# Kernel tuning notes

Measured on AMD Instinct MI355X. Metric: run time of the kernel, lower is better.

## Reference

```python
import jax, jax.numpy as jnp
import numpy as np

WIDTH = 128


def setup_inputs() -> dict:
    key = jax.random.key(0)
    k_logits, k_w1, k_b1, k_w2, k_b2 = jax.random.split(key, 5)
    B, T, V = 32, 256, 4096
    logits = jax.random.normal(k_logits, (B, T, V), dtype=jnp.float32)
    # Linear(1, width): weight [width, 1] -> stored transposed as [1, width]
    w1 = jax.random.normal(k_w1, (1, WIDTH), dtype=jnp.float32) / jnp.sqrt(1.0)
    b1 = jax.random.normal(k_b1, (WIDTH,), dtype=jnp.float32) * 0.1
    # Linear(width, 1): weight [1, width] -> stored transposed as [width, 1]
    w2 = jax.random.normal(k_w2, (WIDTH, 1), dtype=jnp.float32) / jnp.sqrt(WIDTH)
    b2 = jax.random.normal(k_b2, (1,), dtype=jnp.float32) * 0.1
    return {"logits": logits, "w1": w1, "b1": b1, "w2": w2, "b2": b2}


def reference(logits, w1, b1, w2, b2):
    B, T, V = logits.shape
    logits_trim = logits[:, :-1, :]                       # [B, T-1, V]
    # entropy of softmax over the class dim; logits - logsumexp == log_softmax
    logp = jax.nn.log_softmax(logits_trim, axis=-1)       # [B, T-1, V]
    p = jnp.exp(logp)
    entropy = -jnp.sum(p * logp, axis=-1, keepdims=True)  # [B, T-1, 1]
    entropy_max = jnp.log(jnp.asarray(T, dtype=logits.dtype))  # log(num_steps)
    norm = 2.0 * entropy / entropy_max - 1.0              # [B, T-1, 1]
    # tiny 1 -> width -> 1 MLP
    hidden = jax.nn.relu(norm @ w1 + b1)                  # [B, T-1, width]
    lin = (2.0 * hidden) @ w2 + b2                        # [B, T-1, 1]
    # ns = [T-1, T-2, ..., 1]
    ns = jnp.arange(T - 1, 0, -1, dtype=logits.dtype).reshape(1, T - 1, 1)
    flags_trim = jax.nn.sigmoid(lin - jnp.log(ns))        # [B, T-1, 1]
    zeros = jnp.zeros((B, 1, 1), dtype=logits.dtype)
    ones = jnp.ones((B, 1, 1), dtype=logits.dtype)
    flags = jnp.concatenate([zeros, flags_trim, ones], axis=1)  # [B, T+1, 1]
    probabilities = jax.nn.softmax(logits, axis=2)        # [B, T, V]
    residuals = jnp.cumprod(1.0 - flags[:, :-1], axis=1)  # [B, T, 1] survival
    frequencies = probabilities * flags[:, 1:] * residuals  # [B, T, V]
    return frequencies
```

## Files before the change

kernel.cpp:

```cpp
#include <hip/hip_runtime.h>
#include <math.h>

#define T_DIM 256
#define V_DIM 4096
#define WIDTH 128

typedef float floatx4 __attribute__((ext_vector_type(4)));

__device__ __forceinline__ double wave_sum_d(double v) {
#pragma unroll
  for (int o = 32; o > 0; o >>= 1) v += __shfl_xor(v, o);
  return v;
}

__global__ __launch_bounds__(256) void row_stats(
    const float* __restrict__ logits,
    const float* __restrict__ w1, const float* __restrict__ b1,
    const float* __restrict__ w2, const float* __restrict__ b2,
    double* __restrict__ row_Z, double* __restrict__ row_flag) {
  const int wave = threadIdx.x >> 6;
  const int lane = threadIdx.x & 63;
  const int row = blockIdx.x * 4 + wave;
  const int t = row & (T_DIM - 1);

  const float4* src = (const float4*)(logits + (size_t)row * V_DIM);

  float zg[4] = {0.f, 0.f, 0.f, 0.f};
  float sg[4] = {0.f, 0.f, 0.f, 0.f};
#pragma unroll
  for (int k = 0; k < 16; ++k) {
    float4 x = src[lane + k * 64];
    const int g = k & 3;
    float vals[4] = {x.x, x.y, x.z, x.w};
#pragma unroll
    for (int j = 0; j < 4; ++j) {
      float ev = __expf(vals[j]);
      zg[g] += ev;
      sg[g] = fmaf(vals[j], ev, sg[g]);
    }
  }
  double zd = wave_sum_d(((double)zg[0] + (double)zg[1]) +
                         ((double)zg[2] + (double)zg[3]));
  double sd = wave_sum_d(((double)sg[0] + (double)sg[1]) +
                         ((double)sg[2] + (double)sg[3]));

  if (lane == 0) row_Z[row] = zd;

  if (t < T_DIM - 1) {
    double H = (double)__logf((float)zd) - sd / zd;
    double nrm = fma(H, 0.36067376022224085, -1.0);
    double acc = 0.0;
#pragma unroll
    for (int j = lane; j < WIDTH; j += 64) {
      double h = fma(nrm, (double)w1[j], (double)b1[j]);
      h = h > 0.0 ? h : 0.0;
      acc = fma(h, (double)w2[j], acc);
    }
    acc = wave_sum_d(acc);
    if (lane == 0) {
      double lin = 2.0 * acc + (double)b2[0];
      float xx = (float)lin - __logf((float)(T_DIM - 1 - t));
      row_flag[row] = 1.0 / (1.0 + (double)__expf(-xx));
    }
  }
}

__global__ __launch_bounds__(64) void scan_k(
    const double* __restrict__ row_Z, const double* __restrict__ row_flag,
    float* __restrict__ row_scale) {
  const int b = blockIdx.x;
  const int lane = threadIdx.x & 63;
  const double* fb = row_flag + (size_t)b * T_DIM;

  double loc[4];
  double p = 1.0;
#pragma unroll
  for (int j = 0; j < 4; ++j) {
    int t = lane * 4 + j;
    double flag_t = (t == 0) ? 0.0 : fb[t - 1];
    p *= (1.0 - flag_t);
    loc[j] = p;
  }
  double inc = p;
#pragma unroll
  for (int o = 1; o < 64; o <<= 1) {
    double up = __shfl_up(inc, o);
    if (lane >= o) inc *= up;
  }
  double exc = __shfl_up(inc, 1);
  if (lane == 0) exc = 1.0;

#pragma unroll
  for (int j = 0; j < 4; ++j) {
    int t = lane * 4 + j;
    double resid = exc * loc[j];
    double flt = (t == T_DIM - 1) ? 1.0 : fb[t];
    row_scale[(size_t)b * T_DIM + t] =
        (float)(flt * resid / row_Z[(size_t)b * T_DIM + t]);
  }
}

__global__ __launch_bounds__(256) void out_k(const float* __restrict__ logits,
                                             const float* __restrict__ row_scale,
                                             float* __restrict__ out) {
  const int row = blockIdx.x;
  const int tid = threadIdx.x;
  const float sc = row_scale[row];

  const float4* src = (const float4*)(logits + (size_t)row * V_DIM);
  floatx4* dst = (floatx4*)(out + (size_t)row * V_DIM);

#pragma unroll
  for (int k = 0; k < 4; ++k) {
    float4 x = src[tid + k * 256];
    floatx4 o;
    o.x = __expf(x.x) * sc;
    o.y = __expf(x.y) * sc;
    o.z = __expf(x.z) * sc;
    o.w = __expf(x.w) * sc;
    __builtin_nontemporal_store(o, &dst[tid + k * 256]);
  }
}

extern "C" void kernel_launch(void* const* d_in, const int* in_sizes, int n_in,
                              void* d_out, int out_size, void* d_ws, size_t ws_size,
                              hipStream_t stream) {
  const float* logits = (const float*)d_in[0];
  const float* w1 = (const float*)d_in[1];
  const float* b1 = (const float*)d_in[2];
  const float* w2 = (const float*)d_in[3];
  const float* b2 = (const float*)d_in[4];
  float* out = (float*)d_out;

  const size_t nrows = (size_t)in_sizes[0] / V_DIM;
  const size_t nbatch = nrows / T_DIM;

  double* row_Z = (double*)d_ws;
  double* row_flag = row_Z + nrows;
  float* row_scale = (float*)(row_flag + nrows);

  row_stats<<<(int)(nrows / 4), 256, 0, stream>>>(logits, w1, b1, w2, b2,
                                                  row_Z, row_flag);
  scan_k<<<(int)nbatch, 64, 0, stream>>>(row_Z, row_flag, row_scale);
  out_k<<<(int)nrows, 256, 0, stream>>>(logits, row_scale, out);
}
```

Before: 257.3 us.

## Split row reduction across two blocks with atomics and separate flag kernel

The per-row softmax sum and entropy reduction is moved from one wave per row to two 256-thread blocks per row. Each block reduces half the row and atomically adds its partials into zeroed double accumulators. The tiny MLP and flag computation move into a separate kernel. This raises parallelism and memory-level parallelism in the streaming pass, but adds a memset, an extra kernel launch, and double atomics.

```diff
diff --git a/kernel.cpp b/kernel.cpp
--- a/kernel.cpp
+++ b/kernel.cpp
@@ -13,55 +13,79 @@
   return v;
 }
 
-__global__ __launch_bounds__(256) void row_stats(
+__global__ __launch_bounds__(256) void zs_reduce(
     const float* __restrict__ logits,
+    double* __restrict__ row_Z, double* __restrict__ row_S) {
+  const int blk = blockIdx.x;
+  const int row = blk >> 1;
+  const int chunk = blk & 1;
+  const int tid = threadIdx.x;
+  const int lane = tid & 63;
+  const int wave = tid >> 6;
+
+  const float4* src =
+      (const float4*)(logits + (size_t)row * V_DIM) + chunk * 512;
+
+  float4 a = src[tid];
+  float4 b = src[tid + 256];
+
+  float za = 0.f, sa = 0.f, zb = 0.f, sb = 0.f;
+  float va[4] = {a.x, a.y, a.z, a.w};
+  float vb[4] = {b.x, b.y, b.z, b.w};
+#pragma unroll
+  for (int j = 0; j < 4; ++j) {
+    float e = __expf(va[j]);
+    za += e;
+    sa = fmaf(va[j], e, sa);
+  }
+#pragma unroll
+  for (int j = 0; j < 4; ++j) {
+    float e = __expf(vb[j]);
+    zb += e;
+    sb = fmaf(vb[j], e, sb);
+  }
+
+  double zd = wave_sum_d((double)za + (double)zb);
+  double sd = wave_sum_d((double)sa + (double)sb);
+
+  __shared__ double lz[4], ls[4];
+  if (lane == 0) { lz[wave] = zd; ls[wave] = sd; }
+  __syncthreads();
+  if (tid == 0) {
+    double zt = (lz[0] + lz[1]) + (lz[2] + lz[3]);
+    double st = (ls[0] + ls[1]) + (ls[2] + ls[3]);
+    atomicAdd(&row_Z[row], zt);
+    atomicAdd(&row_S[row], st);
+  }
+}
+
+__global__ __launch_bounds__(256) void flag_k(
+    const double* __restrict__ row_Z, const double* __restrict__ row_S,
     const float* __restrict__ w1, const float* __restrict__ b1,
     const float* __restrict__ w2, const float* __restrict__ b2,
-    double* __restrict__ row_Z, double* __restrict__ row_flag) {
+    double* __restrict__ row_flag) {
   const int wave = threadIdx.x >> 6;
   const int lane = threadIdx.x & 63;
   const int row = blockIdx.x * 4 + wave;
   const int t = row & (T_DIM - 1);
+  if (t >= T_DIM - 1) return;
 
-  const float4* src = (const float4*)(logits + (size_t)row * V_DIM);
-
-  float zg[4] = {0.f, 0.f, 0.f, 0.f};
-  float sg[4] = {0.f, 0.f, 0.f, 0.f};
+  const double zd = row_Z[row];
+  const double sd = row_S[row];
+  double H = (double)__logf((float)zd) - sd / zd;
+  double nrm = fma(H, 0.36067376022224085, -1.0);
+  double acc = 0.0;
 #pragma unroll
-  for (int k = 0; k < 16; ++k) {
-    float4 x = src[lane + k * 64];
-    const int g = k & 3;
-    float vals[4] = {x.x, x.y, x.z, x.w};
-#pragma unroll
-    for (int j = 0; j < 4; ++j) {
-      float ev = __expf(vals[j]);
-      zg[g] += ev;
-      sg[g] = fmaf(vals[j], ev, sg[g]);
-    }
+  for (int j = lane; j < WIDTH; j += 64) {
+    double h = fma(nrm, (double)w1[j], (double)b1[j]);
+    h = h > 0.0 ? h : 0.0;
+    acc = fma(h, (double)w2[j], acc);
   }
-  double zd = wave_sum_d(((double)zg[0] + (double)zg[1]) +
-                         ((double)zg[2] + (double)zg[3]));
-  double sd = wave_sum_d(((double)sg[0] + (double)sg[1]) +
-                         ((double)sg[2] + (double)sg[3]));
-
-  if (lane == 0) row_Z[row] = zd;
-
-  if (t < T_DIM - 1) {
-    double H = (double)__logf((float)zd) - sd / zd;
-    double nrm = fma(H, 0.36067376022224085, -1.0);
-    double acc = 0.0;
-#pragma unroll
-    for (int j = lane; j < WIDTH; j += 64) {
-      double h = fma(nrm, (double)w1[j], (double)b1[j]);
-      h = h > 0.0 ? h : 0.0;
-      acc = fma(h, (double)w2[j], acc);
-    }
-    acc = wave_sum_d(acc);
-    if (lane == 0) {
-      double lin = 2.0 * acc + (double)b2[0];
-      float xx = (float)lin - __logf((float)(T_DIM - 1 - t));
-      row_flag[row] = 1.0 / (1.0 + (double)__expf(-xx));
-    }
+  acc = wave_sum_d(acc);
+  if (lane == 0) {
+    double lin = 2.0 * acc + (double)b2[0];
+    float xx = (float)lin - __logf((float)(T_DIM - 1 - t));
+    row_flag[row] = 1.0 / (1.0 + (double)__expf(-xx));
   }
 }
 
@@ -136,11 +160,15 @@
   const size_t nbatch = nrows / T_DIM;
 
   double* row_Z = (double*)d_ws;
-  double* row_flag = row_Z + nrows;
+  double* row_S = row_Z + nrows;
+  double* row_flag = row_S + nrows;
   float* row_scale = (float*)(row_flag + nrows);
 
-  row_stats<<<(int)(nrows / 4), 256, 0, stream>>>(logits, w1, b1, w2, b2,
-                                                  row_Z, row_flag);
+  hipMemsetAsync(row_Z, 0, 2 * nrows * sizeof(double), stream);
+
+  zs_reduce<<<(int)(nrows * 2), 256, 0, stream>>>(logits, row_Z, row_S);
+  flag_k<<<(int)(nrows / 4), 256, 0, stream>>>(row_Z, row_S, w1, b1, w2, b2,
+                                               row_flag);
   scan_k<<<(int)nbatch, 64, 0, stream>>>(row_Z, row_flag, row_scale);
   out_k<<<(int)nrows, 256, 0, stream>>>(logits, row_scale, out);
 }
```

After: 259.2 us. Within noise of the previous version (+0.7%).
